# Kernel tuning notes

Measured on AMD Instinct MI355X. Metric: run time of the kernel, lower is better.

Reference implementation:

```python
import jax, jax.numpy as jnp
import numpy as np

NODE_FEATURES = 256
HIDDEN = 32
N_NODES = 100000
N_EDGES = 3200000


def _glorot(key, shape):
    fan_in, fan_out = shape[-2], shape[-1]
    lim = (6.0 / (fan_in + fan_out)) ** 0.5
    return jax.random.uniform(key, shape, jnp.float32, -lim, lim)


def setup_inputs() -> dict:
    key = jax.random.key(0)
    ks = jax.random.split(key, 12)
    in_cat = NODE_FEATURES + HIDDEN  # DConv input is cat([X, H])
    x = jax.random.normal(ks[0], (N_NODES, NODE_FEATURES), jnp.float32)
    edge_index = jax.random.randint(ks[1], (2, N_EDGES), 0, N_NODES, jnp.int64)
    return {
        "x": x,
        "edge_index": edge_index,
        # DConv weights have shape (2, K=1, in, out); squeeze K -> (2, in, out)
        "w_z": _glorot(ks[2], (2, in_cat, HIDDEN)),
        "b_z": jnp.zeros((HIDDEN,), jnp.float32),
        "w_r": _glorot(ks[3], (2, in_cat, HIDDEN)),
        "b_r": jnp.zeros((HIDDEN,), jnp.float32),
        "w_h": _glorot(ks[4], (2, in_cat, HIDDEN)),
        "b_h": jnp.zeros((HIDDEN,), jnp.float32),
        # fc head, stored as [in, out]
        "fc1_w": _glorot(ks[5], (HIDDEN, HIDDEN)),
        "fc1_b": jnp.zeros((HIDDEN,), jnp.float32),
        "fc2_w": _glorot(ks[6], (HIDDEN, 1)),
        "fc2_b": jnp.zeros((1,), jnp.float32),
    }


def _dconv_k1(inp, w, b):
    # K=1 DConv: only the k=0 Chebyshev term for both diffusion directions,
    # i.e. no propagation over edges. H = X @ W_out + X @ W_in + bias.
    return inp @ (w[0] + w[1]) + b


def reference(x, edge_index, w_z, b_z, w_r, b_r, w_h, b_h, fc1_w, fc1_b, fc2_w, fc2_b):
    n = x.shape[0]
    h0 = jnp.zeros((n, HIDDEN), x.dtype)  # DCRNN called with H=None -> zeros
    xh0 = jnp.concatenate([x, h0], axis=1)  # [N, F+H]
    z = jax.nn.sigmoid(_dconv_k1(xh0, w_z, b_z))  # update gate
    r = jax.nn.sigmoid(_dconv_k1(xh0, w_r, b_r))  # reset gate
    xrh = jnp.concatenate([x, r * h0], axis=1)
    h_tilde = jnp.tanh(_dconv_k1(xrh, w_h, b_h))
    h = z * h0 + (1.0 - z) * h_tilde  # [N, 32]
    # fc head: Linear-ReLU-Dropout(eval=identity)-Linear-Sigmoid
    hidden = jax.nn.relu(h @ fc1_w + fc1_b)
    out = jax.nn.sigmoid(hidden @ fc2_w + fc2_b)  # [N, 1]
    return out
```

## Files before the change

kernel.cpp:

```cpp
#include <hip/hip_runtime.h>
#include <hip/hip_bf16.h>


#define NF     256
#define TILE   32
#define WPB    4
#define MB     (TILE * WPB)
#define NTHR   256
#define NCHUNK 8
#define NBUF   3
#define ABUF   4096

typedef __attribute__((ext_vector_type(8)))  short  short8;
typedef __attribute__((ext_vector_type(16))) float  floatx16;

__device__ __forceinline__ unsigned f2bf(float f) {
    __hip_bfloat16 h = __float2bfloat16(f);
    return (unsigned)*(unsigned short*)&h;
}
__device__ __forceinline__ float fast_sigmoid(float v) {
    return 1.0f / (1.0f + __expf(-v));
}
__device__ __forceinline__ float fast_tanh(float v) {
    return 1.0f - 2.0f / (1.0f + __expf(2.0f * v));
}
__device__ __forceinline__ void dma16(const void* g, void* l) {
    __builtin_amdgcn_global_load_lds(
        (const __attribute__((address_space(1))) unsigned int*)g,
        (__attribute__((address_space(3))) unsigned int*)l,
        16, 0, 0);
}

__global__ void prep_W(const float* __restrict__ wz,
                       const float* __restrict__ wh,
                       unsigned short* __restrict__ Wf)
{
    int idx = blockIdx.x * blockDim.x + threadIdx.x;
    if (idx >= NF * 64) return;
    int j    = idx & 7;
    int lane = (idx >> 3) & 63;
    int nt   = (idx >> 9) & 1;
    int kt   = idx >> 10;
    int k = kt * 16 + (lane >> 5) * 8 + j;
    int o = nt * 32 + (lane & 31);
    const int PLANE = 288 * 32;
    float v;
    if (o < 32) v = wz[k * 32 + o]        + wz[PLANE + k * 32 + o];
    else        v = wh[k * 32 + (o - 32)] + wh[PLANE + k * 32 + (o - 32)];
    Wf[idx] = (unsigned short)f2bf(v);
}

#define ISSUE_CHUNK(cc, buf)                                        \
    do {                                                            \
        dma16(ap0 + (size_t)(cc) * 128, (buf));                     \
        dma16(ap1 + (size_t)(cc) * 128, (buf) + 1024);              \
        dma16(ap2 + (size_t)(cc) * 128, (buf) + 2048);              \
        dma16(ap3 + (size_t)(cc) * 128, (buf) + 3072);              \
    } while (0)

__global__ void __launch_bounds__(NTHR, 2)
rgcn_main(const float* __restrict__ x,
          const unsigned short* __restrict__ Wf,
          const float* __restrict__ bz,
          const float* __restrict__ bh,
          const float* __restrict__ fc1w,
          const float* __restrict__ fc1b,
          const float* __restrict__ fc2w,
          const float* __restrict__ fc2b,
          float* __restrict__ out,
          int n_nodes)
{
    __shared__ __align__(16) char SA [WPB * NBUF * ABUF];
    __shared__ __align__(16) char SBf[32 * 1024];

    const int tid   = threadIdx.x;
    const int lane  = tid & 63;
    const int wave  = tid >> 6;
    const int node0 = blockIdx.x * MB + wave * TILE;

    {
        const char* wsrc = (const char*)Wf;
#pragma unroll
        for (int i = 0; i < 8; ++i) {
            int g = wave * 8 + i;
            dma16(wsrc + (size_t)g * 1024 + lane * 16, SBf + g * 1024);
        }
    }

    const int nc  = lane & 31;
    const float bzn = bz[nc];
    const float bhn = bh[nc];

    asm volatile("s_waitcnt vmcnt(0)" ::: "memory");
    __syncthreads();

    const int rg   = lane >> 3;
    const int gslt = (lane & 7) ^ rg;
    int r0 = node0 +      rg; if (r0 >= n_nodes) r0 = n_nodes - 1;
    int r1 = node0 +  8 + rg; if (r1 >= n_nodes) r1 = n_nodes - 1;
    int r2 = node0 + 16 + rg; if (r2 >= n_nodes) r2 = n_nodes - 1;
    int r3 = node0 + 24 + rg; if (r3 >= n_nodes) r3 = n_nodes - 1;
    const char* ap0 = (const char*)x + (size_t)r0 * (NF * 4) + gslt * 16;
    const char* ap1 = (const char*)x + (size_t)r1 * (NF * 4) + gslt * 16;
    const char* ap2 = (const char*)x + (size_t)r2 * (NF * 4) + gslt * 16;
    const char* ap3 = (const char*)x + (size_t)r3 * (NF * 4) + gslt * 16;
    char* aw = SA + wave * (NBUF * ABUF);

    const int m   = lane & 31;
    const int h   = lane >> 5;
    const int rsw = m & 7;
    const char* bl = SBf + lane * 16;

    ISSUE_CHUNK(0, aw);
    ISSUE_CHUNK(1, aw + ABUF);
    ISSUE_CHUNK(2, aw + 2 * ABUF);

    floatx16 acc0 = {};
    floatx16 acc1 = {};

#pragma unroll
    for (int c = 0; c < NCHUNK; ++c) {
        if (c < 6)       asm volatile("s_waitcnt vmcnt(8)" ::: "memory");
        else if (c == 6) asm volatile("s_waitcnt vmcnt(4)" ::: "memory");
        else             asm volatile("s_waitcnt vmcnt(0)" ::: "memory");
        __builtin_amdgcn_sched_barrier(0);

        char* ab = aw + (c % NBUF) * ABUF;
#pragma unroll
        for (int kk = 0; kk < 2; ++kk) {
            int sA = 4 * kk + 2 * h;
            float4 f0 = *(const float4*)(ab + m * 128 + (((sA    ) ^ rsw) << 4));
            float4 f1 = *(const float4*)(ab + m * 128 + (((sA + 1) ^ rsw) << 4));
            int kt = 2 * c + kk;
            uint4 b0u = *(const uint4*)(bl + (size_t)(2 * kt    ) * 1024);
            uint4 b1u = *(const uint4*)(bl + (size_t)(2 * kt + 1) * 1024);

            union { short8 s; unsigned u[4]; } A, B0, B1;
            A.u[0] = f2bf(f0.x) | (f2bf(f0.y) << 16);
            A.u[1] = f2bf(f0.z) | (f2bf(f0.w) << 16);
            A.u[2] = f2bf(f1.x) | (f2bf(f1.y) << 16);
            A.u[3] = f2bf(f1.z) | (f2bf(f1.w) << 16);
            B0.u[0] = b0u.x; B0.u[1] = b0u.y; B0.u[2] = b0u.z; B0.u[3] = b0u.w;
            B1.u[0] = b1u.x; B1.u[1] = b1u.y; B1.u[2] = b1u.z; B1.u[3] = b1u.w;

            acc0 = __builtin_amdgcn_mfma_f32_32x32x16_bf16(A.s, B0.s, acc0, 0, 0, 0);
            acc1 = __builtin_amdgcn_mfma_f32_32x32x16_bf16(A.s, B1.s, acc1, 0, 0, 0);
        }

        if (c < NCHUNK - NBUF) {
            __builtin_amdgcn_sched_barrier(0);
            ISSUE_CHUNK(c + NBUF, ab);
        }
    }

    float* Hw = (float*)aw;
#pragma unroll
    for (int r = 0; r < 16; ++r) {
        int row = (r & 3) + 8 * (r >> 2) + 4 * (lane >> 5);
        float z = fast_sigmoid(acc0[r] + bzn);
        float t = fast_tanh   (acc1[r] + bhn);
        int boff = row * 128 + ((((nc >> 2) ^ (row & 7)) << 4) | ((nc & 3) << 2));
        *(float*)((char*)Hw + boff) = (1.0f - z) * t;
    }
    asm volatile("s_waitcnt lgkmcnt(0)" ::: "memory");

    const int nl   = lane & 31;
    const int half = lane >> 5;
    float hbuf[32];
#pragma unroll
    for (int q = 0; q < 8; ++q) {
        int boff = nl * 128 + ((q ^ (nl & 7)) << 4);
        float4 v = *(const float4*)((char*)Hw + boff);
        hbuf[q * 4 + 0] = v.x; hbuf[q * 4 + 1] = v.y;
        hbuf[q * 4 + 2] = v.z; hbuf[q * 4 + 3] = v.w;
    }
    float part = 0.0f;
    for (int jj = 0; jj < 16; ++jj) {
        int j = (half << 4) + jj;
        float s = fc1b[j];
#pragma unroll
        for (int o = 0; o < 32; ++o)
            s = fmaf(hbuf[o], fc1w[o * 32 + j], s);
        part = fmaf(fmaxf(s, 0.0f), fc2w[j], part);
    }
    part += __shfl_xor(part, 32);
    if (half == 0) {
        int gn = node0 + nl;
        if (gn < n_nodes)
            out[gn] = fast_sigmoid(part + fc2b[0]);
    }
}

extern "C" void kernel_launch(void* const* d_in, const int* in_sizes, int n_in,
                              void* d_out, int out_size, void* d_ws, size_t ws_size,
                              hipStream_t stream) {
    const float* x    = (const float*)d_in[0];
    const float* wz   = (const float*)d_in[2];
    const float* bz   = (const float*)d_in[3];
    const float* wh   = (const float*)d_in[6];
    const float* bh   = (const float*)d_in[7];
    const float* fc1w = (const float*)d_in[8];
    const float* fc1b = (const float*)d_in[9];
    const float* fc2w = (const float*)d_in[10];
    const float* fc2b = (const float*)d_in[11];
    float* out = (float*)d_out;
    unsigned short* Wf = (unsigned short*)d_ws;

    const int n = in_sizes[0] / NF;

    prep_W<<<(NF * 64 + 255) / 256, 256, 0, stream>>>(wz, wh, Wf);
    rgcn_main<<<(n + MB - 1) / MB, NTHR, 0, stream>>>(
        x, Wf, bz, bh, fc1w, fc1b, fc2w, fc2b, out, n);
}
```

Measured before the change: 201.6 us.

## Prepack x to bf16 MFMA layout in separate kernel and load directly

Adds a repack kernel that converts x from fp32 to bf16 and writes it in the MFMA A-fragment layout in workspace. The main kernel then loads A fragments straight from global memory, dropping the LDS triple-buffer pipeline, and raises the occupancy hint to 5. The goal is to cut LDS use and in-loop conversion work, but it adds a full extra pass over x (read 100 MB fp32, write 50 MB bf16, then read it again). The main kernel also no longer clamps rows for a partial final tile, so reads past the packed region are possible.

```diff
diff --git a/kernel.cpp b/kernel.cpp
--- a/kernel.cpp
+++ b/kernel.cpp
@@ -2,14 +2,11 @@
 #include <hip/hip_bf16.h>
 
 
-#define NF     256
-#define TILE   32
-#define WPB    4
-#define MB     (TILE * WPB)
-#define NTHR   256
-#define NCHUNK 8
-#define NBUF   3
-#define ABUF   4096
+#define NF    256
+#define TILE  32
+#define WPB   4
+#define MB    (TILE * WPB)
+#define NTHR  256
 
 typedef __attribute__((ext_vector_type(8)))  short  short8;
 typedef __attribute__((ext_vector_type(16))) float  floatx16;
@@ -50,16 +47,33 @@
     Wf[idx] = (unsigned short)f2bf(v);
 }
 
-#define ISSUE_CHUNK(cc, buf)                                        \
-    do {                                                            \
-        dma16(ap0 + (size_t)(cc) * 128, (buf));                     \
-        dma16(ap1 + (size_t)(cc) * 128, (buf) + 1024);              \
-        dma16(ap2 + (size_t)(cc) * 128, (buf) + 2048);              \
-        dma16(ap3 + (size_t)(cc) * 128, (buf) + 3072);              \
-    } while (0)
+__global__ void __launch_bounds__(NTHR)
+repack_A(const float* __restrict__ x, unsigned short* __restrict__ Ap,
+         int n_nodes)
+{
+    const int total = n_nodes * 64;
+    for (int i = blockIdx.x * blockDim.x + threadIdx.x; i < total;
+         i += gridDim.x * blockDim.x) {
+        int row = i >> 6;
+        int q   = i & 63;
+        float4 v = ((const float4*)x)[i];
+        unsigned lo = f2bf(v.x) | (f2bf(v.y) << 16);
+        unsigned hi = f2bf(v.z) | (f2bf(v.w) << 16);
+        int k0   = q << 2;
+        int tile = row >> 7;
+        int wv   = (row >> 5) & 3;
+        int m    = row & 31;
+        int kt   = k0 >> 4;
+        int h    = (k0 >> 3) & 1;
+        int e    = k0 & 7;
+        size_t base = ((size_t)(tile * 4 + wv) * 16 + kt) * 512
+                      + (size_t)(m + 32 * h) * 8 + e;
+        *(uint2*)(Ap + base) = make_uint2(lo, hi);
+    }
+}
 
-__global__ void __launch_bounds__(NTHR, 2)
-rgcn_main(const float* __restrict__ x,
+__global__ void __launch_bounds__(NTHR, 5)
+rgcn_main(const unsigned short* __restrict__ Ap,
           const unsigned short* __restrict__ Wf,
           const float* __restrict__ bz,
           const float* __restrict__ bh,
@@ -70,7 +84,6 @@
           float* __restrict__ out,
           int n_nodes)
 {
-    __shared__ __align__(16) char SA [WPB * NBUF * ABUF];
     __shared__ __align__(16) char SBf[32 * 1024];
 
     const int tid   = threadIdx.x;
@@ -86,7 +99,6 @@
             dma16(wsrc + (size_t)g * 1024 + lane * 16, SBf + g * 1024);
         }
     }
-
     const int nc  = lane & 31;
     const float bzn = bz[nc];
     const float bhn = bh[nc];
@@ -94,66 +106,28 @@
     asm volatile("s_waitcnt vmcnt(0)" ::: "memory");
     __syncthreads();
 
-    const int rg   = lane >> 3;
-    const int gslt = (lane & 7) ^ rg;
-    int r0 = node0 +      rg; if (r0 >= n_nodes) r0 = n_nodes - 1;
-    int r1 = node0 +  8 + rg; if (r1 >= n_nodes) r1 = n_nodes - 1;
-    int r2 = node0 + 16 + rg; if (r2 >= n_nodes) r2 = n_nodes - 1;
-    int r3 = node0 + 24 + rg; if (r3 >= n_nodes) r3 = n_nodes - 1;
-    const char* ap0 = (const char*)x + (size_t)r0 * (NF * 4) + gslt * 16;
-    const char* ap1 = (const char*)x + (size_t)r1 * (NF * 4) + gslt * 16;
-    const char* ap2 = (const char*)x + (size_t)r2 * (NF * 4) + gslt * 16;
-    const char* ap3 = (const char*)x + (size_t)r3 * (NF * 4) + gslt * 16;
-    char* aw = SA + wave * (NBUF * ABUF);
-
-    const int m   = lane & 31;
-    const int h   = lane >> 5;
-    const int rsw = m & 7;
+    const unsigned short* aw =
+        Ap + ((size_t)(blockIdx.x * WPB + wave) * 16) * 512 + lane * 8;
     const char* bl = SBf + lane * 16;
-
-    ISSUE_CHUNK(0, aw);
-    ISSUE_CHUNK(1, aw + ABUF);
-    ISSUE_CHUNK(2, aw + 2 * ABUF);
 
     floatx16 acc0 = {};
     floatx16 acc1 = {};
 
 #pragma unroll
-    for (int c = 0; c < NCHUNK; ++c) {
-        if (c < 6)       asm volatile("s_waitcnt vmcnt(8)" ::: "memory");
-        else if (c == 6) asm volatile("s_waitcnt vmcnt(4)" ::: "memory");
-        else             asm volatile("s_waitcnt vmcnt(0)" ::: "memory");
-        __builtin_amdgcn_sched_barrier(0);
-
-        char* ab = aw + (c % NBUF) * ABUF;
-#pragma unroll
-        for (int kk = 0; kk < 2; ++kk) {
-            int sA = 4 * kk + 2 * h;
-            float4 f0 = *(const float4*)(ab + m * 128 + (((sA    ) ^ rsw) << 4));
-            float4 f1 = *(const float4*)(ab + m * 128 + (((sA + 1) ^ rsw) << 4));
-            int kt = 2 * c + kk;
-            uint4 b0u = *(const uint4*)(bl + (size_t)(2 * kt    ) * 1024);
-            uint4 b1u = *(const uint4*)(bl + (size_t)(2 * kt + 1) * 1024);
-
-            union { short8 s; unsigned u[4]; } A, B0, B1;
-            A.u[0] = f2bf(f0.x) | (f2bf(f0.y) << 16);
-            A.u[1] = f2bf(f0.z) | (f2bf(f0.w) << 16);
-            A.u[2] = f2bf(f1.x) | (f2bf(f1.y) << 16);
-            A.u[3] = f2bf(f1.z) | (f2bf(f1.w) << 16);
-            B0.u[0] = b0u.x; B0.u[1] = b0u.y; B0.u[2] = b0u.z; B0.u[3] = b0u.w;
-            B1.u[0] = b1u.x; B1.u[1] = b1u.y; B1.u[2] = b1u.z; B1.u[3] = b1u.w;
-
-            acc0 = __builtin_amdgcn_mfma_f32_32x32x16_bf16(A.s, B0.s, acc0, 0, 0, 0);
-            acc1 = __builtin_amdgcn_mfma_f32_32x32x16_bf16(A.s, B1.s, acc1, 0, 0, 0);
-        }
-
-        if (c < NCHUNK - NBUF) {
-            __builtin_amdgcn_sched_barrier(0);
-            ISSUE_CHUNK(c + NBUF, ab);
-        }
+    for (int kt = 0; kt < 16; ++kt) {
+        short8 a = *(const short8*)(aw + (size_t)kt * 512);
+        uint4 b0u = *(const uint4*)(bl + (size_t)(2 * kt    ) * 1024);
+        uint4 b1u = *(const uint4*)(bl + (size_t)(2 * kt + 1) * 1024);
+        union { short8 s; unsigned u[4]; } B0, B1;
+        B0.u[0] = b0u.x; B0.u[1] = b0u.y; B0.u[2] = b0u.z; B0.u[3] = b0u.w;
+        B1.u[0] = b1u.x; B1.u[1] = b1u.y; B1.u[2] = b1u.z; B1.u[3] = b1u.w;
+        acc0 = __builtin_amdgcn_mfma_f32_32x32x16_bf16(a, B0.s, acc0, 0, 0, 0);
+        acc1 = __builtin_amdgcn_mfma_f32_32x32x16_bf16(a, B1.s, acc1, 0, 0, 0);
     }
 
-    float* Hw = (float*)aw;
+    __syncthreads();
+
+    float* Hw = (float*)(SBf + wave * 8192);
 #pragma unroll
     for (int r = 0; r < 16; ++r) {
         int row = (r & 3) + 8 * (r >> 2) + 4 * (lane >> 5);
@@ -204,11 +178,14 @@
     const float* fc2w = (const float*)d_in[10];
     const float* fc2b = (const float*)d_in[11];
     float* out = (float*)d_out;
+
     unsigned short* Wf = (unsigned short*)d_ws;
+    unsigned short* Ap = (unsigned short*)((char*)d_ws + 65536);
 
     const int n = in_sizes[0] / NF;
 
-    prep_W<<<(NF * 64 + 255) / 256, 256, 0, stream>>>(wz, wh, Wf);
+    prep_W  <<<(NF * 64 + 255) / 256, 256, 0, stream>>>(wz, wh, Wf);
+    repack_A<<<2048, NTHR, 0, stream>>>(x, Ap, n);
     rgcn_main<<<(n + MB - 1) / MB, NTHR, 0, stream>>>(
-        x, Wf, bz, bh, fc1w, fc1b, fc2w, fc2b, out, n);
+        Ap, Wf, bz, bh, fc1w, fc1b, fc2w, fc2b, out, n);
 }
```

Result: slower. 236.5 us (+17.3%).
